# Kernel optimization log

Measured on AMD Instinct MI355X. Metric: run time of the kernel, lower is better.

The kernel has to match this reference:

```python
import jax, jax.numpy as jnp
import numpy as np

WIDTH = 1024
NUM_HEADS = 16
HEAD_DIM = WIDTH // NUM_HEADS  # 64
WINDOW = 256
BATCH = 2
SEQ = 2048
_MIN_LOGITS_VALUE = -1e30


def setup_inputs() -> dict:
    key = jax.random.key(0)
    ks = jax.random.split(key, 6)
    std = 1.0 / np.sqrt(WIDTH)
    x = jax.random.normal(ks[0], (BATCH, SEQ, WIDTH), dtype=jnp.float32)
    Wq = jax.random.normal(ks[1], (WIDTH, WIDTH), dtype=jnp.float32) * std
    Wk = jax.random.normal(ks[2], (HEAD_DIM, WIDTH), dtype=jnp.float32) * std
    Wv = jax.random.normal(ks[3], (HEAD_DIM, WIDTH), dtype=jnp.float32) * std
    Wf = jax.random.normal(ks[4], (WIDTH, WIDTH), dtype=jnp.float32) * std  # variance_scale=1.0
    bf = jnp.zeros((WIDTH,), dtype=jnp.float32)
    return {"x": x, "Wq": Wq, "Wk": Wk, "Wv": Wv, "Wf": Wf, "bf": bf}


def reference(x, Wq, Wk, Wv, Wf, bf):
    b, t, _ = x.shape
    # projections (torch Linear: y = x @ W.T)
    q = (x @ Wq.T).reshape(b, t, NUM_HEADS, HEAD_DIM)  # b t n h
    k = x @ Wk.T  # b t h  (MQA: single shared key head)
    v = x @ Wv.T  # b t h
    scale = 1.0 / np.sqrt(HEAD_DIM)
    # logits: queries per-head against the shared key head
    logits = jnp.einsum('btnh,bsh->bnts', q, k) * scale  # b n t s
    # symmetric local window mask |i - j| <= WINDOW
    pos = jnp.arange(t)
    mask = jnp.abs(pos[:, None] - pos[None, :]) <= WINDOW  # t s
    masked = jnp.where(mask[None, None, :, :], logits, _MIN_LOGITS_VALUE)
    probs = jax.nn.softmax(masked.astype(jnp.float32), axis=-1).astype(logits.dtype)
    out = jnp.einsum('bnts,bsh->btnh', probs, v).reshape(b, t, WIDTH)
    return out @ Wf.T + bf
```

## Files before the change

### kernel.cpp

```cpp
#include <hip/hip_runtime.h>

typedef __bf16 bf16;
typedef __bf16 bf16x8 __attribute__((ext_vector_type(8)));
typedef float  f32x4  __attribute__((ext_vector_type(4)));

#define MFMA(a, b, c) __builtin_amdgcn_mfma_f32_16x16x32_bf16((a), (b), (c), 0, 0, 0)

static constexpr int B_   = 2;
static constexpr int T_   = 2048;
static constexpr int D_   = 1024;
static constexpr int NH_  = 16;
static constexpr int HD_  = 64;
static constexpr int WIN_ = 256;
static constexpr int M_   = B_ * T_;
static constexpr int NQKV = D_ + 2 * HD_;

__device__ __forceinline__ void gld_lds16(const bf16* g, bf16* l) {
  __builtin_amdgcn_global_load_lds(
      (const __attribute__((address_space(1))) void*)g,
      (__attribute__((address_space(3))) void*)l, 16, 0, 0);
}

__global__ __launch_bounds__(256) void conv_all(
    const float* __restrict__ x,  const float* __restrict__ wq,
    const float* __restrict__ wk, const float* __restrict__ wv,
    const float* __restrict__ wf, const float* __restrict__ bv,
    bf16* __restrict__ xc, bf16* __restrict__ wqkv,
    bf16* __restrict__ wfc, bf16* __restrict__ bfc) {
  const long i = (long)(blockIdx.x * 256 + threadIdx.x) * 4;
  const float* src; bf16* dst; long off;
  if      (i < 4194304L) { src = x;  dst = xc;              off = 0; }
  else if (i < 5242880L) { src = wq; dst = wqkv;            off = 4194304L; }
  else if (i < 5308416L) { src = wk; dst = wqkv + 1048576L; off = 5242880L; }
  else if (i < 5373952L) { src = wv; dst = wqkv + 1114112L; off = 5308416L; }
  else if (i < 6422528L) { src = wf; dst = wfc;             off = 5373952L; }
  else if (i < 6423552L) { src = bv; dst = bfc;             off = 6422528L; }
  else return;
  const long j = i - off;
  const float4 v = *(const float4*)(src + j);
  bf16 o[4] = {(bf16)v.x, (bf16)v.y, (bf16)v.z, (bf16)v.w};
  *(uint2*)(dst + j) = *(const uint2*)o;
}

template <int EPI>
__global__ __launch_bounds__(256) void gemm64x128(
    const bf16* __restrict__ A, const bf16* __restrict__ Bw,
    void* __restrict__ Cout, const bf16* __restrict__ bias,
    bf16* __restrict__ kb, bf16* __restrict__ vT, int N, int K) {
  __shared__ __align__(16) bf16 As[64 * 64];
  __shared__ __align__(16) bf16 Bs[128 * 64];

  const int tid  = threadIdx.x;
  const int w    = tid >> 6;
  const int lane = tid & 63;
  const int quad = lane >> 4;
  const int l16  = lane & 15;
  const int wm   = w & 1;
  const int wn   = w >> 1;
  const int m0   = blockIdx.x * 64;
  const int n0   = blockIdx.y * 128;
  const int lrow = lane >> 3;
  const int lcol = (lane & 7) * 8;

  f32x4 acc[2][4] = {};

  for (int k0 = 0; k0 < K; k0 += 64) {
    __syncthreads();
#pragma unroll
    for (int t = 0; t < 6; ++t) {
      const int inst = w * 6 + t;
      if (inst < 8) {
        gld_lds16(&A[(size_t)(m0 + inst * 8 + lrow) * K + k0 + lcol],
                  &As[inst * 512]);
      } else {
        const int bi = inst - 8;
        gld_lds16(&Bw[(size_t)(n0 + bi * 8 + lrow) * K + k0 + lcol],
                  &Bs[bi * 512]);
      }
    }
    __syncthreads();
#pragma unroll
    for (int kk = 0; kk < 64; kk += 32) {
      bf16x8 a[2], b[4];
#pragma unroll
      for (int i = 0; i < 2; ++i)
        a[i] = *(const bf16x8*)&As[(wm * 32 + i * 16 + l16) * 64 + kk + quad * 8];
#pragma unroll
      for (int j = 0; j < 4; ++j)
        b[j] = *(const bf16x8*)&Bs[(wn * 64 + j * 16 + l16) * 64 + kk + quad * 8];
#pragma unroll
      for (int i = 0; i < 2; ++i)
#pragma unroll
        for (int j = 0; j < 4; ++j) acc[i][j] = MFMA(a[i], b[j], acc[i][j]);
    }
  }

#pragma unroll
  for (int i = 0; i < 2; ++i) {
#pragma unroll
    for (int j = 0; j < 4; ++j) {
      const int col     = n0 + wn * 64 + j * 16 + l16;
      const int rowbase = m0 + wm * 32 + i * 16 + quad * 4;
      if (EPI == 1) {
        if (col < D_) {
          bf16* qb = (bf16*)Cout;
#pragma unroll
          for (int r = 0; r < 4; ++r)
            qb[(size_t)(rowbase + r) * D_ + col] = (bf16)acc[i][j][r];
        } else if (col < D_ + HD_) {
#pragma unroll
          for (int r = 0; r < 4; ++r)
            kb[(size_t)(rowbase + r) * HD_ + (col - D_)] = (bf16)acc[i][j][r];
        } else {
          bf16 o[4] = {(bf16)acc[i][j][0], (bf16)acc[i][j][1],
                       (bf16)acc[i][j][2], (bf16)acc[i][j][3]};
          *(uint2*)&vT[(size_t)(col - D_ - HD_) * M_ + rowbase] = *(const uint2*)o;
        }
      } else {
        float* outp = (float*)Cout;
        const float bvv = (float)bias[col];
#pragma unroll
        for (int r = 0; r < 4; ++r)
          outp[(size_t)(rowbase + r) * D_ + col] = acc[i][j][r] + bvv;
      }
    }
  }
}

__global__ __launch_bounds__(256) void attn_win128(
    const bf16* __restrict__ q, const bf16* __restrict__ k,
    const bf16* __restrict__ vT, bf16* __restrict__ o) {
  __shared__ __align__(16) bf16 Qs[128 * 64];
  __shared__ __align__(16) bf16 Ks[64 * 64];
  __shared__ __align__(16) bf16 Vt[64 * 64];
  __shared__ __align__(16) bf16 Ps[128 * 72];

  const int tid  = threadIdx.x;
  const int w    = tid >> 6;
  const int lane = tid & 63;
  const int quad = lane >> 4;
  const int l16  = lane & 15;
  const int lrow = lane >> 3;
  const int lcol = (lane & 7) * 8;

  const int t0 = blockIdx.x * 128;
  const int n  = blockIdx.y;
  const int b  = blockIdx.z;
  const float scale = 0.125f;

#pragma unroll
  for (int t = 0; t < 4; ++t) {
    const int inst = w * 4 + t;
    gld_lds16(&q[((size_t)(b * T_ + t0 + inst * 8 + lrow)) * D_ + n * HD_ + lcol],
              &Qs[inst * 512]);
  }

  f32x4 o_acc[2][4] = {};
  float l_r[2][4] = {};

  for (int st = t0 - WIN_; st <= t0 + WIN_ + 64; st += 64) {
    if (st < 0 || st >= T_) continue;

    __syncthreads();
#pragma unroll
    for (int t = 0; t < 2; ++t) {
      const int inst = w * 2 + t;
      gld_lds16(&k[((size_t)(b * T_ + st + inst * 8 + lrow)) * HD_ + lcol],
                &Ks[inst * 512]);
      gld_lds16(&vT[(size_t)(inst * 8 + lrow) * M_ + b * T_ + st + lcol],
                &Vt[inst * 512]);
    }
    __syncthreads();

    f32x4 sacc[2][4] = {};
#pragma unroll
    for (int kk = 0; kk < 64; kk += 32) {
      bf16x8 aq[2];
#pragma unroll
      for (int rg = 0; rg < 2; ++rg)
        aq[rg] = *(const bf16x8*)&Qs[(w * 32 + rg * 16 + l16) * 64 + kk + quad * 8];
#pragma unroll
      for (int nt = 0; nt < 4; ++nt) {
        bf16x8 bk = *(const bf16x8*)&Ks[(nt * 16 + l16) * 64 + kk + quad * 8];
#pragma unroll
        for (int rg = 0; rg < 2; ++rg) sacc[rg][nt] = MFMA(aq[rg], bk, sacc[rg][nt]);
      }
    }

#pragma unroll
    for (int rg = 0; rg < 2; ++rg) {
#pragma unroll
      for (int r = 0; r < 4; ++r) {
        const int t = t0 + w * 32 + rg * 16 + quad * 4 + r;
#pragma unroll
        for (int nt = 0; nt < 4; ++nt) {
          const int s = st + nt * 16 + l16;
          const int d = t - s;
          float sv = fminf(sacc[rg][nt][r] * scale, 30.0f);
          float p = (d > WIN_ || d < -WIN_) ? 0.0f : __expf(sv);
          l_r[rg][r] += p;
          Ps[(w * 32 + rg * 16 + quad * 4 + r) * 72 + nt * 16 + l16] = (bf16)p;
        }
      }
    }
    __syncthreads();

#pragma unroll
    for (int kk = 0; kk < 64; kk += 32) {
      bf16x8 ap[2];
#pragma unroll
      for (int rg = 0; rg < 2; ++rg)
        ap[rg] = *(const bf16x8*)&Ps[(w * 32 + rg * 16 + l16) * 72 + kk + quad * 8];
#pragma unroll
      for (int nt = 0; nt < 4; ++nt) {
        bf16x8 bv = *(const bf16x8*)&Vt[(nt * 16 + l16) * 64 + kk + quad * 8];
#pragma unroll
        for (int rg = 0; rg < 2; ++rg)
          o_acc[rg][nt] = MFMA(ap[rg], bv, o_acc[rg][nt]);
      }
    }
  }

#pragma unroll
  for (int rg = 0; rg < 2; ++rg)
#pragma unroll
    for (int r = 0; r < 4; ++r)
#pragma unroll
      for (int off = 1; off < 16; off <<= 1)
        l_r[rg][r] += __shfl_xor(l_r[rg][r], off);

#pragma unroll
  for (int rg = 0; rg < 2; ++rg) {
#pragma unroll
    for (int nt = 0; nt < 4; ++nt) {
#pragma unroll
      for (int r = 0; r < 4; ++r) {
        const int t = t0 + w * 32 + rg * 16 + quad * 4 + r;
        const int h = nt * 16 + l16;
        o[((size_t)(b * T_ + t)) * D_ + n * HD_ + h] =
            (bf16)(o_acc[rg][nt][r] / (l_r[rg][r] + 1e-30f));
      }
    }
  }
}

extern "C" void kernel_launch(void* const* d_in, const int* in_sizes, int n_in,
                              void* d_out, int out_size, void* d_ws, size_t ws_size,
                              hipStream_t stream) {
  float* out = (float*)d_out;

  bf16* xc   = (bf16*)d_ws;
  bf16* wqkv = xc   + (size_t)M_ * D_;
  bf16* wfc  = wqkv + (size_t)NQKV * D_;
  bf16* bfc  = wfc  + (size_t)D_ * D_;
  bf16* qb   = bfc  + D_;
  bf16* kb   = qb   + (size_t)M_ * D_;
  bf16* vT   = kb   + (size_t)M_ * HD_;

  dim3 blk(256);
  conv_all<<<dim3((6423552 / 4 + 255) / 256), blk, 0, stream>>>(
      (const float*)d_in[0], (const float*)d_in[1], (const float*)d_in[2],
      (const float*)d_in[3], (const float*)d_in[4], (const float*)d_in[5],
      xc, wqkv, wfc, bfc);

  gemm64x128<1><<<dim3(M_ / 64, NQKV / 128), blk, 0, stream>>>(
      xc, wqkv, (void*)qb, nullptr, kb, vT, NQKV, D_);

  attn_win128<<<dim3(T_ / 128, NH_, B_), blk, 0, stream>>>(qb, kb, vT, qb);

  gemm64x128<2><<<dim3(M_ / 64, D_ / 128), blk, 0, stream>>>(
      qb, wfc, (void*)out, bfc, nullptr, nullptr, D_, D_);
}
```

Before: 159.5 us.

## Double-buffer K/V tiles in attention, fold softmax scale into Q, skip interior masking

The attention kernel now keeps two K/V shared-memory buffers. The next 64-key tile is prefetched while the current tile's QK^T and softmax run, and the loop bounds are clamped so out-of-range tiles are never visited. The 1/sqrt(d) scale moves into the Q projection epilogue. Tiles lying fully inside the window skip the per-element mask test. This overlaps global-to-LDS latency with compute and trims ALU work, at the cost of extra LDS use, which may reduce occupancy.

After: 158.7 us. About the same (-0.5%).

```diff
diff --git a/kernel.cpp b/kernel.cpp
--- a/kernel.cpp
+++ b/kernel.cpp
@@ -106,7 +106,7 @@
           bf16* qb = (bf16*)Cout;
 #pragma unroll
           for (int r = 0; r < 4; ++r)
-            qb[(size_t)(rowbase + r) * D_ + col] = (bf16)acc[i][j][r];
+            qb[(size_t)(rowbase + r) * D_ + col] = (bf16)(acc[i][j][r] * 0.125f);
         } else if (col < D_ + HD_) {
 #pragma unroll
           for (int r = 0; r < 4; ++r)
@@ -131,8 +131,8 @@
     const bf16* __restrict__ q, const bf16* __restrict__ k,
     const bf16* __restrict__ vT, bf16* __restrict__ o) {
   __shared__ __align__(16) bf16 Qs[128 * 64];
-  __shared__ __align__(16) bf16 Ks[64 * 64];
-  __shared__ __align__(16) bf16 Vt[64 * 64];
+  __shared__ __align__(16) bf16 Ks[2][64 * 64];
+  __shared__ __align__(16) bf16 Vt[2][64 * 64];
   __shared__ __align__(16) bf16 Ps[128 * 72];
 
   const int tid  = threadIdx.x;
@@ -146,7 +146,6 @@
   const int t0 = blockIdx.x * 128;
   const int n  = blockIdx.y;
   const int b  = blockIdx.z;
-  const float scale = 0.125f;
 
 #pragma unroll
   for (int t = 0; t < 4; ++t) {
@@ -155,22 +154,29 @@
               &Qs[inst * 512]);
   }
 
-  f32x4 o_acc[2][4] = {};
-  float l_r[2][4] = {};
-
-  for (int st = t0 - WIN_; st <= t0 + WIN_ + 64; st += 64) {
-    if (st < 0 || st >= T_) continue;
-
-    __syncthreads();
+  auto stageKV = [&](int st, int pb) {
 #pragma unroll
     for (int t = 0; t < 2; ++t) {
       const int inst = w * 2 + t;
       gld_lds16(&k[((size_t)(b * T_ + st + inst * 8 + lrow)) * HD_ + lcol],
-                &Ks[inst * 512]);
+                &Ks[pb][inst * 512]);
       gld_lds16(&vT[(size_t)(inst * 8 + lrow) * M_ + b * T_ + st + lcol],
-                &Vt[inst * 512]);
-    }
-    __syncthreads();
+                &Vt[pb][inst * 512]);
+    }
+  };
+
+  const int st_lo = (t0 - WIN_ > 0) ? t0 - WIN_ : 0;
+  const int st_hi = (t0 + WIN_ + 64 < T_ - 64) ? t0 + WIN_ + 64 : T_ - 64;
+
+  stageKV(st_lo, 0);
+  int pb = 0;
+
+  f32x4 o_acc[2][4] = {};
+  float l_r[2][4] = {};
+
+  for (int st = st_lo; st <= st_hi; st += 64) {
+    __syncthreads();
+    if (st + 64 <= st_hi) stageKV(st + 64, pb ^ 1);
 
     f32x4 sacc[2][4] = {};
 #pragma unroll
@@ -181,27 +187,44 @@
         aq[rg] = *(const bf16x8*)&Qs[(w * 32 + rg * 16 + l16) * 64 + kk + quad * 8];
 #pragma unroll
       for (int nt = 0; nt < 4; ++nt) {
-        bf16x8 bk = *(const bf16x8*)&Ks[(nt * 16 + l16) * 64 + kk + quad * 8];
+        bf16x8 bk = *(const bf16x8*)&Ks[pb][(nt * 16 + l16) * 64 + kk + quad * 8];
 #pragma unroll
         for (int rg = 0; rg < 2; ++rg) sacc[rg][nt] = MFMA(aq[rg], bk, sacc[rg][nt]);
       }
     }
 
-#pragma unroll
-    for (int rg = 0; rg < 2; ++rg) {
-#pragma unroll
-      for (int r = 0; r < 4; ++r) {
-        const int t = t0 + w * 32 + rg * 16 + quad * 4 + r;
-#pragma unroll
-        for (int nt = 0; nt < 4; ++nt) {
-          const int s = st + nt * 16 + l16;
-          const int d = t - s;
-          float sv = fminf(sacc[rg][nt][r] * scale, 30.0f);
-          float p = (d > WIN_ || d < -WIN_) ? 0.0f : __expf(sv);
-          l_r[rg][r] += p;
-          Ps[(w * 32 + rg * 16 + quad * 4 + r) * 72 + nt * 16 + l16] = (bf16)p;
+    const int off_t = st - t0;
+    const bool need_mask =
+        (off_t < w * 32 - (WIN_ - 31)) || (off_t > w * 32 + (WIN_ - 63));
+    if (!need_mask) {
+#pragma unroll
+      for (int rg = 0; rg < 2; ++rg)
+#pragma unroll
+        for (int r = 0; r < 4; ++r) {
+#pragma unroll
+          for (int nt = 0; nt < 4; ++nt) {
+            const float p = __expf(fminf(sacc[rg][nt][r], 30.0f));
+            l_r[rg][r] += p;
+            Ps[(w * 32 + rg * 16 + quad * 4 + r) * 72 + nt * 16 + l16] = (bf16)p;
+          }
         }
-      }
+    } else {
+#pragma unroll
+      for (int rg = 0; rg < 2; ++rg)
+#pragma unroll
+        for (int r = 0; r < 4; ++r) {
+          const int t = t0 + w * 32 + rg * 16 + quad * 4 + r;
+#pragma unroll
+          for (int nt = 0; nt < 4; ++nt) {
+            const int s = st + nt * 16 + l16;
+            const int d = t - s;
+            float p = (d > WIN_ || d < -WIN_)
+                          ? 0.0f
+                          : __expf(fminf(sacc[rg][nt][r], 30.0f));
+            l_r[rg][r] += p;
+            Ps[(w * 32 + rg * 16 + quad * 4 + r) * 72 + nt * 16 + l16] = (bf16)p;
+          }
+        }
     }
     __syncthreads();
 
@@ -213,12 +236,13 @@
         ap[rg] = *(const bf16x8*)&Ps[(w * 32 + rg * 16 + l16) * 72 + kk + quad * 8];
 #pragma unroll
       for (int nt = 0; nt < 4; ++nt) {
-        bf16x8 bv = *(const bf16x8*)&Vt[(nt * 16 + l16) * 64 + kk + quad * 8];
+        bf16x8 bv = *(const bf16x8*)&Vt[pb][(nt * 16 + l16) * 64 + kk + quad * 8];
 #pragma unroll
         for (int rg = 0; rg < 2; ++rg)
           o_acc[rg][nt] = MFMA(ap[rg], bv, o_acc[rg][nt]);
       }
     }
+    pb ^= 1;
   }
 
 #pragma unroll
```
